# Performance work log

Measured on AMD Instinct MI355X. Metric: run time of the kernel, lower is better.

The kernel has to match this reference:

```python
import jax, jax.numpy as jnp
import numpy as np
import math

NUM_HEADS = 16

def get_slopes(n):
    def pow2(n):
        start = 2 ** (-2 ** (-(math.log2(n) - 3)))
        return [start * start ** i for i in range(n)]
    if math.log2(n).is_integer():
        return pow2(n)
    c = 2 ** math.floor(math.log2(n))
    return pow2(c) + get_slopes(2 * c)[0::2][: n - c]


def setup_inputs() -> dict:
    key = jax.random.key(0)
    ks = jax.random.split(key, 5)
    B, T, C = 2, 2048, 1024
    return {
        "x": jax.random.normal(ks[0], (B, T, C), dtype=jnp.float32),
        "W_qkv": jax.random.normal(ks[1], (C, 3 * C), dtype=jnp.float32) * 0.02,
        "b_qkv": jax.random.normal(ks[2], (3 * C,), dtype=jnp.float32) * 0.02,
        "W_proj": jax.random.normal(ks[3], (C, C), dtype=jnp.float32) * 0.02,
        "b_proj": jax.random.normal(ks[4], (C,), dtype=jnp.float32) * 0.02,
    }


def reference(x, W_qkv, b_qkv, W_proj, b_proj):
    B, T, C = x.shape
    H = NUM_HEADS
    D = C // H
    qkv = x @ W_qkv + b_qkv                       # [B,T,3C]
    q, k, v = jnp.split(qkv, 3, axis=-1)
    q = q.reshape(B, T, H, D).transpose(0, 2, 1, 3)  # [B,H,T,D]
    k = k.reshape(B, T, H, D).transpose(0, 2, 1, 3)
    v = v.reshape(B, T, H, D).transpose(0, 2, 1, 3)

    slopes = jnp.asarray(get_slopes(H), dtype=jnp.float32)  # [H]
    idx = jnp.arange(T)
    # alibi_bias(L).T in source: -(i-j) for j<=i, 0 for j>i  == min(j-i, 0)
    alibi = jnp.minimum(idx[None, :] - idx[:, None], 0).astype(jnp.float32)  # [T,T]
    bias = slopes[:, None, None] * alibi          # [H,T,T]

    scale = 1.0 / math.sqrt(D)
    scores = jnp.einsum("bhtd,bhsd->bhts", q, k) * scale + bias[None]
    # NOTE: source code builds a causal -inf mask but never adds it -> non-causal
    w = jax.nn.softmax(scores, axis=-1)
    y = jnp.einsum("bhts,bhsd->bhtd", w, v)       # [B,H,T,D]
    y = y.transpose(0, 2, 1, 3).reshape(B, T, C)
    return y @ W_proj + b_proj
```

## Files before the change

### kernel.cpp

```cpp
#include <hip/hip_runtime.h>
#include <hip/hip_bf16.h>
#include <cmath>
#include <cstdint>

typedef __bf16 bf16_t;
typedef __bf16 bf16x8 __attribute__((ext_vector_type(8)));
typedef float f32x4 __attribute__((ext_vector_type(4)));
typedef float f32x8 __attribute__((ext_vector_type(8)));
typedef float f32x16 __attribute__((ext_vector_type(16)));
typedef unsigned int u32x2 __attribute__((ext_vector_type(2)));
typedef unsigned int u32x4 __attribute__((ext_vector_type(4)));

static_assert(sizeof(bf16x8) == 16, "bf16x8 must be 16B");

#define MFMA16(a, b, c) __builtin_amdgcn_mfma_f32_16x16x32_bf16((a), (b), (c), 0, 0, 0)
#define MFMA32(a, b, c) __builtin_amdgcn_mfma_f32_32x32x16_bf16((a), (b), (c), 0, 0, 0)

__device__ __forceinline__ void load_lds_16B(const bf16_t* gsrc, bf16_t* ldst) {
  __builtin_amdgcn_global_load_lds(
      (const __attribute__((address_space(1))) void*)gsrc,
      (__attribute__((address_space(3))) void*)ldst, 16, 0, 0);
}

__global__ void detect_dtype(const unsigned short* __restrict__ x,
                             int* __restrict__ flag) {
  const int lane = threadIdx.x;
  int cnt = 0;
#pragma unroll
  for (int t = 0; t < 8; ++t) {
    unsigned short u = x[2 * (lane + 64 * t)];
    int e = (u >> 7) & 0xFF;
    cnt += (e >= 90 && e <= 130) ? 1 : 0;
  }
#pragma unroll
  for (int off = 1; off < 64; off <<= 1) cnt += __shfl_xor(cnt, off, 64);
  if (lane == 0) *flag = (cnt < 300) ? 1 : 0;
}

__global__ __launch_bounds__(256) void convert_x(const void* __restrict__ x_,
                                                 bf16_t* __restrict__ xb,
                                                 const int* __restrict__ flagp) {
  const size_t idx = ((size_t)blockIdx.x * 256 + threadIdx.x) * 8;
  if (*flagp) {
    f32x8 v = *(const f32x8*)((const float*)x_ + idx);
    bf16x8 bv;
#pragma unroll
    for (int e = 0; e < 8; ++e) bv[e] = (bf16_t)v[e];
    *(bf16x8*)&xb[idx] = bv;
  } else {
    *(bf16x8*)&xb[idx] = *(const bf16x8*)((const bf16_t*)x_ + idx);
  }
}

__global__ __launch_bounds__(256) void wt_transpose(const void* __restrict__ W_,
                                                    bf16_t* __restrict__ Wt,
                                                    int K, int N,
                                                    const int* __restrict__ flagp) {
  __shared__ bf16_t tile[64 * 72];
  const int is_f32 = *flagp;
  const int tid = threadIdx.x;
  const int k0 = blockIdx.y * 64;
  const int n0 = blockIdx.x * 64;
  const int r = tid >> 3;
  const int c = (tid & 7) * 8;
#pragma unroll
  for (int t = 0; t < 2; ++t) {
    int rr = r + t * 32;
    if (is_f32) {
      const float* W = (const float*)W_;
      f32x8 v = *(const f32x8*)&W[(size_t)(k0 + rr) * N + n0 + c];
      bf16x8 bv;
#pragma unroll
      for (int e = 0; e < 8; ++e) bv[e] = (bf16_t)v[e];
      *(bf16x8*)&tile[rr * 72 + c] = bv;
    } else {
      const bf16_t* W = (const bf16_t*)W_;
      *(bf16x8*)&tile[rr * 72 + c] = *(const bf16x8*)&W[(size_t)(k0 + rr) * N + n0 + c];
    }
  }
  __syncthreads();
#pragma unroll
  for (int t = 0; t < 2; ++t) {
    int rr = r + t * 32;
    bf16x8 v;
#pragma unroll
    for (int e = 0; e < 8; ++e) v[e] = tile[(c + e) * 72 + rr];
    *(bf16x8*)&Wt[(size_t)(n0 + rr) * K + k0 + c] = v;
  }
}

__global__ __launch_bounds__(256, 2) void gemm_bt(
    const bf16_t* __restrict__ A, const bf16_t* __restrict__ Bt,
    const void* __restrict__ bias_, void* __restrict__ C_,
    bf16_t* __restrict__ qb, bf16_t* __restrict__ kb, bf16_t* __restrict__ vt,
    int M, int N, int K, int mode, const int* __restrict__ flagp) {
  __shared__ bf16_t As[128 * 64];
  __shared__ bf16_t Bs[128 * 64];
  const int is_f32 = *flagp;
  const int tid = threadIdx.x;
  const int wave = tid >> 6, lane = tid & 63;
  const int l16 = lane & 15, quad = lane >> 4;
  const int m0 = blockIdx.y * 128, n0 = blockIdx.x * 128;
  const int wm = (wave >> 1) * 64, wn = (wave & 1) * 64;
  const int lr = lane >> 3, lc = (lane & 7) * 8;
  f32x4 acc[4][4] = {};

  for (int k0 = 0; k0 < K; k0 += 64) {
#pragma unroll
    for (int t = 0; t < 4; ++t) {
      const int chunk = wave * 4 + t;
      const int row = chunk * 8 + lr;
      load_lds_16B(&A[(size_t)(m0 + row) * K + k0 + lc], &As[chunk * 512]);
      load_lds_16B(&Bt[(size_t)(n0 + row) * K + k0 + lc], &Bs[chunk * 512]);
    }
    __syncthreads();
#pragma unroll
    for (int ks = 0; ks < 2; ++ks) {
      bf16x8 af[4], bfr[4];
#pragma unroll
      for (int i = 0; i < 4; ++i) {
        af[i]  = *(const bf16x8*)&As[(wm + i * 16 + l16) * 64 + ks * 32 + quad * 8];
        bfr[i] = *(const bf16x8*)&Bs[(wn + i * 16 + l16) * 64 + ks * 32 + quad * 8];
      }
#pragma unroll
      for (int i = 0; i < 4; ++i)
#pragma unroll
        for (int j = 0; j < 4; ++j)
          acc[i][j] = MFMA16(af[i], bfr[j], acc[i][j]);
    }
    __syncthreads();
  }

#pragma unroll
  for (int j = 0; j < 4; ++j) {
    const int n = n0 + wn + j * 16 + l16;
    const float bv = is_f32 ? ((const float*)bias_)[n]
                            : (float)((const bf16_t*)bias_)[n];
    if (mode == 0) {
#pragma unroll
      for (int i = 0; i < 4; ++i)
#pragma unroll
        for (int r = 0; r < 4; ++r) {
          int m = m0 + wm + i * 16 + quad * 4 + r;
          float val = acc[i][j][r] + bv;
          if (is_f32) ((float*)C_)[(size_t)m * N + n] = val;
          else ((bf16_t*)C_)[(size_t)m * N + n] = (bf16_t)val;
        }
    } else {
      const int region = n >> 10;
      const int nn = n & 1023;
      const int hh = nn >> 6, dd = nn & 63;
#pragma unroll
      for (int i = 0; i < 4; ++i)
#pragma unroll
        for (int r = 0; r < 4; ++r) {
          int m = m0 + wm + i * 16 + quad * 4 + r;
          int bb = m >> 11, tt = m & 2047;
          size_t bh = (size_t)(bb * 16 + hh);
          float val = acc[i][j][r] + bv;
          if (region == 0)
            qb[(bh * 2048 + tt) * 64 + dd] = (bf16_t)val;
          else if (region == 1)
            kb[(bh * 2048 + tt) * 64 + dd] = (bf16_t)val;
          else
            vt[bh * 131072 + (size_t)dd * 2048 + tt] = (bf16_t)val;
        }
    }
  }
}

__global__ __launch_bounds__(512, 4) void attn_kernel(
    const bf16_t* __restrict__ qbuf, const bf16_t* __restrict__ kbuf,
    const bf16_t* __restrict__ vT, bf16_t* __restrict__ y) {
  const int T = 2048;
  __shared__ __align__(16) char smem[65536];
  bf16_t* KsA = (bf16_t*)smem;
  bf16_t* VsA = (bf16_t*)(smem + 32768);

  const int tid = threadIdx.x;
  const int wave = tid >> 6, lane = tid & 63;
  const int g2 = wave >> 2, wp = wave & 3;
  const int l32 = lane & 31, hi = lane >> 5;
  const int x7 = l32 & 7;
  const int bh = blockIdx.y;
  const int b = bh >> 4, h = bh & 15;
  const int i0 = blockIdx.x * 128 + wp * 32;
  const float L2E = 1.44269504088896f;
  const float c1 = 0.125f * L2E;
  const float c2 = exp2f(-0.5f * (float)(h + 1)) * L2E;

  bf16x8 qf[4];
  {
    const bf16_t* qrow = qbuf + ((size_t)bh * T + i0 + l32) * 64 + hi * 8;
#pragma unroll
    for (int kk = 0; kk < 4; ++kk) qf[kk] = *(const bf16x8*)&qrow[kk * 16];
  }

  f32x16 o[2] = {};
  float rsum = 0.f;

  const bf16_t* kbase = kbuf + (size_t)bh * T * 64;
  const bf16_t* vbase = vT + (size_t)bh * 64 * T;
  bf16_t* Kg = KsA + g2 * 8192;
  bf16_t* Vg = VsA + g2 * 8192;

  const int jbase = g2 * 1024;
  const float dif = (float)(4 * hi - i0 - l32);

  const int lr8 = lane >> 3;
  const int swz = ((lane & 7) ^ lr8) * 8;
  const bf16_t* kl0 = kbase + (size_t)(jbase + wp * 16 + lr8) * 64 + swz;
  const bf16_t* kl1 = kl0 + 8 * 64;
  const bf16_t* vl0 = vbase + (size_t)(wp * 16 + lr8) * T + jbase + swz;
  const bf16_t* vl1 = vl0 + (size_t)8 * T;
  bf16_t* kd0 = Kg + wp * 1024;
  bf16_t* vd0 = Vg + wp * 1024;

#define STAGE(bufsel, trel)                                         \
  do {                                                              \
    const size_t ko_ = (size_t)(trel) * 4096;                       \
    const size_t vo_ = (size_t)(trel) * 64;                         \
    bf16_t* kd_ = kd0 + (bufsel) * 4096;                            \
    bf16_t* vd_ = vd0 + (bufsel) * 4096;                            \
    load_lds_16B(kl0 + ko_, kd_);                                   \
    load_lds_16B(kl1 + ko_, kd_ + 512);                             \
    load_lds_16B(vl0 + vo_, vd_);                                   \
    load_lds_16B(vl1 + vo_, vd_ + 512);                             \
  } while (0)

  STAGE(0, 0);
  __asm__ volatile("s_waitcnt vmcnt(0)" ::: "memory");
  __syncthreads();

  for (int t = 0; t < 16; ++t) {
    const int cur = t & 1;
    const int j0 = jbase + t * 64;

    if (t < 15) STAGE(cur ^ 1, t + 1);

    const bf16_t* myKs = Kg + cur * 4096;
    const bf16_t* myVs = Vg + cur * 4096;

#pragma unroll
    for (int hl = 0; hl < 2; ++hl) {
      const int jblk = j0 + hl * 32;
      bf16x8 kf[4];
#pragma unroll
      for (int kk = 0; kk < 4; ++kk) {
        const int R = hl * 32 + l32;
        kf[kk] = *(const bf16x8*)&myKs[R * 64 + (((kk << 1) + hi) ^ x7) * 8];
      }
      f32x16 s = {};
      __builtin_amdgcn_s_setprio(1);
#pragma unroll
      for (int kk = 0; kk < 4; ++kk) s = MFMA32(kf[kk], qf[kk], s);
      __builtin_amdgcn_s_setprio(0);

      float rs = 0.f;
      if (jblk >= i0 + 31) {
#pragma unroll
        for (int r = 0; r < 16; ++r) {
          float p = exp2f(c1 * s[r]);
          rs += p; s[r] = p;
        }
      } else {
        const float cjb = c2 * ((float)jblk + dif);
        if (jblk + 31 <= i0) {
#pragma unroll
          for (int r = 0; r < 16; ++r) {
            const float kr = (float)((r & 3) + 8 * (r >> 2));
            float p = exp2f(fmaf(c1, s[r], fmaf(c2, kr, cjb)));
            rs += p; s[r] = p;
          }
        } else {
#pragma unroll
          for (int r = 0; r < 16; ++r) {
            const float kr = (float)((r & 3) + 8 * (r >> 2));
            float p = exp2f(fmaf(c1, s[r], fminf(fmaf(c2, kr, cjb), 0.f)));
            rs += p; s[r] = p;
          }
        }
      }
      rsum += rs;

      unsigned int w[8];
#pragma unroll
      for (int q = 0; q < 8; ++q)
        asm("v_cvt_pk_bf16_f32 %0, %1, %2"
            : "=v"(w[q]) : "v"(s[2 * q]), "v"(s[2 * q + 1]));
      u32x2 q02 = __builtin_amdgcn_permlane32_swap(w[0], w[2], false, false);
      u32x2 q13 = __builtin_amdgcn_permlane32_swap(w[1], w[3], false, false);
      u32x2 q46 = __builtin_amdgcn_permlane32_swap(w[4], w[6], false, false);
      u32x2 q57 = __builtin_amdgcn_permlane32_swap(w[5], w[7], false, false);
      u32x4 a0u = {q02[0], q13[0], q02[1], q13[1]};
      u32x4 a1u = {q46[0], q57[0], q46[1], q57[1]};
      bf16x8 af0 = __builtin_bit_cast(bf16x8, a0u);
      bf16x8 af1 = __builtin_bit_cast(bf16x8, a1u);

      bf16x8 vf[4];
#pragma unroll
      for (int db = 0; db < 2; ++db) {
        const int D = db * 32 + l32;
        vf[db * 2]     = *(const bf16x8*)&myVs[D * 64 + ((hl * 4 + hi) ^ x7) * 8];
        vf[db * 2 + 1] = *(const bf16x8*)&myVs[D * 64 + ((hl * 4 + 2 + hi) ^ x7) * 8];
      }
      __builtin_amdgcn_s_setprio(1);
#pragma unroll
      for (int db = 0; db < 2; ++db) {
        o[db] = MFMA32(af0, vf[db * 2], o[db]);
        o[db] = MFMA32(af1, vf[db * 2 + 1], o[db]);
      }
      __builtin_amdgcn_s_setprio(0);
    }

    __asm__ volatile("s_waitcnt vmcnt(0)" ::: "memory");
    __syncthreads();
  }
#undef STAGE

  rsum += __shfl_xor(rsum, 32, 64);

  float* exO = (float*)smem;
  float* exR = (float*)(smem + 33280);
  if (g2 == 1) {
    float* myO = exO + wp * (32 * 65);
#pragma unroll
    for (int db = 0; db < 2; ++db)
#pragma unroll
      for (int r = 0; r < 16; ++r) {
        const int row = (r & 3) + 8 * (r >> 2) + 4 * hi;
        myO[row * 65 + db * 32 + l32] = o[db][r];
      }
    if (lane < 32) exR[wp * 32 + lane] = rsum;
  }
  __syncthreads();
  if (g2 == 0) {
    float* myO = exO + wp * (32 * 65);
#pragma unroll
    for (int r = 0; r < 16; ++r) {
      const int row = (r & 3) + 8 * (r >> 2) + 4 * hi;
      const float denom = __shfl(rsum, row, 64) + exR[wp * 32 + row];
      const float rden = 1.0f / denom;
      const int ig = i0 + row;
#pragma unroll
      for (int db = 0; db < 2; ++db) {
        const float val = (o[db][r] + myO[row * 65 + db * 32 + l32]) * rden;
        y[((size_t)(b * 2048 + ig)) * 1024 + h * 64 + db * 32 + l32] = (bf16_t)val;
      }
    }
  }
}

extern "C" void kernel_launch(void* const* d_in, const int* in_sizes, int n_in,
                              void* d_out, int out_size, void* d_ws, size_t ws_size,
                              hipStream_t stream) {
  const void* x     = d_in[0];
  const void* Wqkv  = d_in[1];
  const void* bqkv  = d_in[2];
  const void* Wproj = d_in[3];
  const void* bproj = d_in[4];

  const size_t SEG = (size_t)32 * 2048 * 64;
  bf16_t* ws = (bf16_t*)d_ws;
  bf16_t* qb = ws;
  bf16_t* kb = ws + SEG;
  bf16_t* vt = ws + 2 * SEG;
  bf16_t* yb = ws + 3 * SEG;
  bf16_t* WqkvT  = yb;
  bf16_t* WprojT = qb;
  bf16_t* xb = (bf16_t*)d_out;
  int* flag1 = (int*)((char*)d_ws + (size_t)31 * 1024 * 1024);
  int* flag2 = (int*)((char*)d_ws + (size_t)4 * 1024 * 1024);

  detect_dtype<<<1, 64, 0, stream>>>((const unsigned short*)x, flag1);
  wt_transpose<<<dim3(48, 16), 256, 0, stream>>>(Wqkv, WqkvT, 1024, 3072, flag1);
  convert_x<<<2048, 256, 0, stream>>>(x, xb, flag1);
  gemm_bt<<<dim3(24, 32), 256, 0, stream>>>(xb, WqkvT, bqkv, nullptr, qb, kb, vt,
                                            4096, 3072, 1024, 1, flag1);
  attn_kernel<<<dim3(16, 32), 512, 0, stream>>>(qb, kb, vt, yb);
  detect_dtype<<<1, 64, 0, stream>>>((const unsigned short*)x, flag2);
  wt_transpose<<<dim3(16, 16), 256, 0, stream>>>(Wproj, WprojT, 1024, 1024, flag2);
  gemm_bt<<<dim3(8, 32), 256, 0, stream>>>(yb, WprojT, bproj, d_out,
                                           nullptr, nullptr, nullptr,
                                           4096, 1024, 1024, 0, flag2);
}
```

Before: 220.0 us.

## Vectorize GEMM epilogue stores via swapped MFMA operands and LDS-staged V transpose

In the GEMM, swaps the MFMA operand order for the projection and Q/K regions so each lane holds four consecutive output columns, which lets the epilogue write bf16x4/f32x4 vectors instead of scalar stores. The V region instead stages the tile transposed in LDS and writes 16-byte rows into the transposed V buffer, replacing strided scalar writes. In attention, the per-register ALiBi term is precomputed as exp2 factors so the off-diagonal path does one FMA plus a multiply. This adds some LDS and a barrier in the V path, and the factored exponential could change rounding slightly.

```diff
diff --git a/kernel.cpp b/kernel.cpp
--- a/kernel.cpp
+++ b/kernel.cpp
@@ -4,6 +4,7 @@
 #include <cstdint>
 
 typedef __bf16 bf16_t;
+typedef __bf16 bf16x4 __attribute__((ext_vector_type(4)));
 typedef __bf16 bf16x8 __attribute__((ext_vector_type(8)));
 typedef float f32x4 __attribute__((ext_vector_type(4)));
 typedef float f32x8 __attribute__((ext_vector_type(8)));
@@ -94,8 +95,9 @@
     const void* __restrict__ bias_, void* __restrict__ C_,
     bf16_t* __restrict__ qb, bf16_t* __restrict__ kb, bf16_t* __restrict__ vt,
     int M, int N, int K, int mode, const int* __restrict__ flagp) {
-  __shared__ bf16_t As[128 * 64];
-  __shared__ bf16_t Bs[128 * 64];
+  __shared__ __align__(16) char gsm[34816];
+  bf16_t* As = (bf16_t*)gsm;
+  bf16_t* Bs = (bf16_t*)(gsm + 16384);
   const int is_f32 = *flagp;
   const int tid = threadIdx.x;
   const int wave = tid >> 6, lane = tid & 63;
@@ -103,6 +105,7 @@
   const int m0 = blockIdx.y * 128, n0 = blockIdx.x * 128;
   const int wm = (wave >> 1) * 64, wn = (wave & 1) * 64;
   const int lr = lane >> 3, lc = (lane & 7) * 8;
+  const bool swapcd = (mode == 0) || (n0 < 2048);
   f32x4 acc[4][4] = {};
 
   for (int k0 = 0; k0 < K; k0 += 64) {
@@ -122,49 +125,108 @@
         af[i]  = *(const bf16x8*)&As[(wm + i * 16 + l16) * 64 + ks * 32 + quad * 8];
         bfr[i] = *(const bf16x8*)&Bs[(wn + i * 16 + l16) * 64 + ks * 32 + quad * 8];
       }
-#pragma unroll
-      for (int i = 0; i < 4; ++i)
-#pragma unroll
-        for (int j = 0; j < 4; ++j)
-          acc[i][j] = MFMA16(af[i], bfr[j], acc[i][j]);
+      if (swapcd) {
+#pragma unroll
+        for (int i = 0; i < 4; ++i)
+#pragma unroll
+          for (int j = 0; j < 4; ++j)
+            acc[i][j] = MFMA16(bfr[j], af[i], acc[i][j]);
+      } else {
+#pragma unroll
+        for (int i = 0; i < 4; ++i)
+#pragma unroll
+          for (int j = 0; j < 4; ++j)
+            acc[i][j] = MFMA16(af[i], bfr[j], acc[i][j]);
+      }
     }
     __syncthreads();
   }
 
-#pragma unroll
-  for (int j = 0; j < 4; ++j) {
-    const int n = n0 + wn + j * 16 + l16;
-    const float bv = is_f32 ? ((const float*)bias_)[n]
-                            : (float)((const bf16_t*)bias_)[n];
-    if (mode == 0) {
-#pragma unroll
-      for (int i = 0; i < 4; ++i)
-#pragma unroll
-        for (int r = 0; r < 4; ++r) {
-          int m = m0 + wm + i * 16 + quad * 4 + r;
-          float val = acc[i][j][r] + bv;
-          if (is_f32) ((float*)C_)[(size_t)m * N + n] = val;
-          else ((bf16_t*)C_)[(size_t)m * N + n] = (bf16_t)val;
+  if (mode == 0) {
+#pragma unroll
+    for (int j = 0; j < 4; ++j) {
+      const int nb = n0 + wn + j * 16 + quad * 4;
+      float bv[4];
+      if (is_f32) {
+        f32x4 t = *(const f32x4*)((const float*)bias_ + nb);
+#pragma unroll
+        for (int r = 0; r < 4; ++r) bv[r] = t[r];
+      } else {
+        const bf16_t* bp = (const bf16_t*)bias_;
+#pragma unroll
+        for (int r = 0; r < 4; ++r) bv[r] = (float)bp[nb + r];
+      }
+#pragma unroll
+      for (int i = 0; i < 4; ++i) {
+        const int m = m0 + wm + i * 16 + l16;
+        if (is_f32) {
+          f32x4 v;
+#pragma unroll
+          for (int r = 0; r < 4; ++r) v[r] = acc[i][j][r] + bv[r];
+          *(f32x4*)&((float*)C_)[(size_t)m * N + nb] = v;
+        } else {
+          bf16x4 v;
+#pragma unroll
+          for (int r = 0; r < 4; ++r) v[r] = (bf16_t)(acc[i][j][r] + bv[r]);
+          *(bf16x4*)&((bf16_t*)C_)[(size_t)m * N + nb] = v;
         }
-    } else {
-      const int region = n >> 10;
-      const int nn = n & 1023;
+      }
+    }
+  } else if (swapcd) {
+#pragma unroll
+    for (int j = 0; j < 4; ++j) {
+      const int nb = n0 + wn + j * 16 + quad * 4;
+      const int nn = nb & 1023;
+      const int hh = nn >> 6, ddb = nn & 63;
+      bf16_t* outp = ((nb >> 10) == 0) ? qb : kb;
+      float bv[4];
+      if (is_f32) {
+        f32x4 t = *(const f32x4*)((const float*)bias_ + nb);
+#pragma unroll
+        for (int r = 0; r < 4; ++r) bv[r] = t[r];
+      } else {
+        const bf16_t* bp = (const bf16_t*)bias_;
+#pragma unroll
+        for (int r = 0; r < 4; ++r) bv[r] = (float)bp[nb + r];
+      }
+#pragma unroll
+      for (int i = 0; i < 4; ++i) {
+        const int m = m0 + wm + i * 16 + l16;
+        const int bb = m >> 11, tt = m & 2047;
+        bf16x4 v;
+#pragma unroll
+        for (int r = 0; r < 4; ++r) v[r] = (bf16_t)(acc[i][j][r] + bv[r]);
+        *(bf16x4*)&outp[((size_t)(bb * 16 + hh) * 2048 + tt) * 64 + ddb] = v;
+      }
+    }
+  } else {
+    bf16_t* Ct = (bf16_t*)gsm;
+#pragma unroll
+    for (int j = 0; j < 4; ++j) {
+      const int nl = wn + j * 16 + l16;
+      const int n = n0 + nl;
+      const float bvj = is_f32 ? ((const float*)bias_)[n]
+                               : (float)((const bf16_t*)bias_)[n];
+#pragma unroll
+      for (int i = 0; i < 4; ++i) {
+        const int mlb = wm + i * 16 + quad * 4;
+        bf16x4 v;
+#pragma unroll
+        for (int r = 0; r < 4; ++r) v[r] = (bf16_t)(acc[i][j][r] + bvj);
+        *(bf16x4*)&Ct[nl * 136 + mlb] = v;
+      }
+    }
+    __syncthreads();
+    const int t4 = tid >> 4, mc = tid & 15;
+    const int bb = m0 >> 11, ttb = (m0 & 2047) + mc * 8;
+    const int nn0 = n0 & 1023;
+#pragma unroll
+    for (int c = 0; c < 8; ++c) {
+      const int nl = c * 16 + t4;
+      const int nn = nn0 + nl;
       const int hh = nn >> 6, dd = nn & 63;
-#pragma unroll
-      for (int i = 0; i < 4; ++i)
-#pragma unroll
-        for (int r = 0; r < 4; ++r) {
-          int m = m0 + wm + i * 16 + quad * 4 + r;
-          int bb = m >> 11, tt = m & 2047;
-          size_t bh = (size_t)(bb * 16 + hh);
-          float val = acc[i][j][r] + bv;
-          if (region == 0)
-            qb[(bh * 2048 + tt) * 64 + dd] = (bf16_t)val;
-          else if (region == 1)
-            kb[(bh * 2048 + tt) * 64 + dd] = (bf16_t)val;
-          else
-            vt[bh * 131072 + (size_t)dd * 2048 + tt] = (bf16_t)val;
-        }
+      bf16x8 v = *(const bf16x8*)&Ct[nl * 136 + mc * 8];
+      *(bf16x8*)&vt[(size_t)(bb * 16 + hh) * 131072 + (size_t)dd * 2048 + ttb] = v;
     }
   }
 }
@@ -189,6 +251,11 @@
   const float c1 = 0.125f * L2E;
   const float c2 = exp2f(-0.5f * (float)(h + 1)) * L2E;
 
+  float er[16];
+#pragma unroll
+  for (int r = 0; r < 16; ++r)
+    er[r] = exp2f(c2 * (float)((r & 3) + 8 * (r >> 2)));
+
   bf16x8 qf[4];
   {
     const bf16_t* qrow = qbuf + ((size_t)bh * T + i0 + l32) * 64 + hi * 8;
@@ -268,8 +335,7 @@
         if (jblk + 31 <= i0) {
 #pragma unroll
           for (int r = 0; r < 16; ++r) {
-            const float kr = (float)((r & 3) + 8 * (r >> 2));
-            float p = exp2f(fmaf(c1, s[r], fmaf(c2, kr, cjb)));
+            float p = exp2f(fmaf(c1, s[r], cjb)) * er[r];
             rs += p; s[r] = p;
           }
         } else {
```

Result: slower. 229.4 us (+4.3%).

## Prescale Q by softmax constant, factor ALiBi exp, add narrow-tile output projection GEMM

Applied to the files above, without the earlier changes.

The QKV GEMM epilogue now multiplies Q by scale*log2(e), so the attention kernel no longer multiplies each score by c1 before exp2. In the fully-below-diagonal case the per-row ALiBi term is precomputed as er[r]=exp2(c2*kr), so each element needs one add, one exp2 and one multiply. The output projection now uses a new 128x64-tile GEMM kernel that launches twice as many blocks, to fill the CUs better. Rounding Q to bf16 after scaling and multiplying by a separate factor changes numerics slightly.

```diff
diff --git a/kernel.cpp b/kernel.cpp
--- a/kernel.cpp
+++ b/kernel.cpp
@@ -15,6 +15,8 @@
 
 #define MFMA16(a, b, c) __builtin_amdgcn_mfma_f32_16x16x32_bf16((a), (b), (c), 0, 0, 0)
 #define MFMA32(a, b, c) __builtin_amdgcn_mfma_f32_32x32x16_bf16((a), (b), (c), 0, 0, 0)
+
+#define QSCALE 0.18033688011112042f
 
 __device__ __forceinline__ void load_lds_16B(const bf16_t* gsrc, bf16_t* ldst) {
   __builtin_amdgcn_global_load_lds(
@@ -150,6 +152,7 @@
       const int region = n >> 10;
       const int nn = n & 1023;
       const int hh = nn >> 6, dd = nn & 63;
+      const float qs = (region == 0) ? QSCALE : 1.0f;
 #pragma unroll
       for (int i = 0; i < 4; ++i)
 #pragma unroll
@@ -157,7 +160,7 @@
           int m = m0 + wm + i * 16 + quad * 4 + r;
           int bb = m >> 11, tt = m & 2047;
           size_t bh = (size_t)(bb * 16 + hh);
-          float val = acc[i][j][r] + bv;
+          float val = (acc[i][j][r] + bv) * qs;
           if (region == 0)
             qb[(bh * 2048 + tt) * 64 + dd] = (bf16_t)val;
           else if (region == 1)
@@ -166,6 +169,70 @@
             vt[bh * 131072 + (size_t)dd * 2048 + tt] = (bf16_t)val;
         }
     }
+  }
+}
+
+__global__ __launch_bounds__(256, 2) void gemm_bt64(
+    const bf16_t* __restrict__ A, const bf16_t* __restrict__ Bt,
+    const void* __restrict__ bias_, void* __restrict__ C_,
+    int M, int N, int K, const int* __restrict__ flagp) {
+  __shared__ bf16_t As[128 * 64];
+  __shared__ bf16_t Bs[64 * 64];
+  const int is_f32 = *flagp;
+  const int tid = threadIdx.x;
+  const int wave = tid >> 6, lane = tid & 63;
+  const int l16 = lane & 15, quad = lane >> 4;
+  const int m0 = blockIdx.y * 128, n0 = blockIdx.x * 64;
+  const int wm = wave * 32;
+  const int lr = lane >> 3, lc = (lane & 7) * 8;
+  f32x4 acc[2][4] = {};
+
+  for (int k0 = 0; k0 < K; k0 += 64) {
+#pragma unroll
+    for (int t = 0; t < 4; ++t) {
+      const int chunk = wave * 4 + t;
+      const int row = chunk * 8 + lr;
+      load_lds_16B(&A[(size_t)(m0 + row) * K + k0 + lc], &As[chunk * 512]);
+    }
+#pragma unroll
+    for (int t = 0; t < 2; ++t) {
+      const int chunk = wave * 2 + t;
+      const int row = chunk * 8 + lr;
+      load_lds_16B(&Bt[(size_t)(n0 + row) * K + k0 + lc], &Bs[chunk * 512]);
+    }
+    __syncthreads();
+#pragma unroll
+    for (int ks = 0; ks < 2; ++ks) {
+      bf16x8 af[2], bfr[4];
+#pragma unroll
+      for (int i = 0; i < 2; ++i)
+        af[i] = *(const bf16x8*)&As[(wm + i * 16 + l16) * 64 + ks * 32 + quad * 8];
+#pragma unroll
+      for (int j = 0; j < 4; ++j)
+        bfr[j] = *(const bf16x8*)&Bs[(j * 16 + l16) * 64 + ks * 32 + quad * 8];
+#pragma unroll
+      for (int i = 0; i < 2; ++i)
+#pragma unroll
+        for (int j = 0; j < 4; ++j)
+          acc[i][j] = MFMA16(af[i], bfr[j], acc[i][j]);
+    }
+    __syncthreads();
+  }
+
+#pragma unroll
+  for (int j = 0; j < 4; ++j) {
+    const int n = n0 + j * 16 + l16;
+    const float bv = is_f32 ? ((const float*)bias_)[n]
+                            : (float)((const bf16_t*)bias_)[n];
+#pragma unroll
+    for (int i = 0; i < 2; ++i)
+#pragma unroll
+      for (int r = 0; r < 4; ++r) {
+        int m = m0 + wm + i * 16 + quad * 4 + r;
+        float val = acc[i][j][r] + bv;
+        if (is_f32) ((float*)C_)[(size_t)m * N + n] = val;
+        else ((bf16_t*)C_)[(size_t)m * N + n] = (bf16_t)val;
+      }
   }
 }
 
@@ -186,8 +253,12 @@
   const int b = bh >> 4, h = bh & 15;
   const int i0 = blockIdx.x * 128 + wp * 32;
   const float L2E = 1.44269504088896f;
-  const float c1 = 0.125f * L2E;
   const float c2 = exp2f(-0.5f * (float)(h + 1)) * L2E;
+
+  float er[16];
+#pragma unroll
+  for (int r = 0; r < 16; ++r)
+    er[r] = exp2f(c2 * (float)((r & 3) + 8 * (r >> 2)));
 
   bf16x8 qf[4];
   {
@@ -260,7 +331,7 @@
       if (jblk >= i0 + 31) {
 #pragma unroll
         for (int r = 0; r < 16; ++r) {
-          float p = exp2f(c1 * s[r]);
+          float p = exp2f(s[r]);
           rs += p; s[r] = p;
         }
       } else {
@@ -268,15 +339,14 @@
         if (jblk + 31 <= i0) {
 #pragma unroll
           for (int r = 0; r < 16; ++r) {
-            const float kr = (float)((r & 3) + 8 * (r >> 2));
-            float p = exp2f(fmaf(c1, s[r], fmaf(c2, kr, cjb)));
+            float p = exp2f(s[r] + cjb) * er[r];
             rs += p; s[r] = p;
           }
         } else {
 #pragma unroll
           for (int r = 0; r < 16; ++r) {
             const float kr = (float)((r & 3) + 8 * (r >> 2));
-            float p = exp2f(fmaf(c1, s[r], fminf(fmaf(c2, kr, cjb), 0.f)));
+            float p = exp2f(s[r] + fminf(fmaf(c2, kr, cjb), 0.f));
             rs += p; s[r] = p;
           }
         }
@@ -380,7 +450,6 @@
   attn_kernel<<<dim3(16, 32), 512, 0, stream>>>(qb, kb, vt, yb);
   detect_dtype<<<1, 64, 0, stream>>>((const unsigned short*)x, flag2);
   wt_transpose<<<dim3(16, 16), 256, 0, stream>>>(Wproj, WprojT, 1024, 1024, flag2);
-  gemm_bt<<<dim3(8, 32), 256, 0, stream>>>(yb, WprojT, bproj, d_out,
-                                           nullptr, nullptr, nullptr,
-                                           4096, 1024, 1024, 0, flag2);
-}
+  gemm_bt64<<<dim3(16, 32), 256, 0, stream>>>(yb, WprojT, bproj, d_out,
+                                              4096, 1024, 1024, flag2);
+}
```

Result: faster. 214.7 us (-2.4%).
